# Kernel optimization log

Hardware: AMD Instinct MI355X
Metric: run time of the kernel (lower is better)

## Reference

```python
import jax, jax.numpy as jnp
import numpy as np


def setup_inputs() -> dict:
    key = jax.random.key(0)
    k1, k2, k3 = jax.random.split(key, 3)
    B, N, D = 512, 65536, 1          # batch, flattened heatmap locations (256x256), tag_dim
    P, K = 30, 17                    # max people, joints per person (COCO)
    tags = jax.random.normal(k1, (B, N, D), dtype=jnp.float32)
    idx = jax.random.randint(k2, (B, P, K), 0, N, dtype=jnp.int64)
    flag = (jax.random.uniform(k3, (B, P, K)) < 0.9).astype(jnp.int64)
    keypoints = jnp.stack([idx, flag], axis=-1)  # [B,P,K,2]
    return {"tags": tags, "keypoints": keypoints}


def reference(tags, keypoints):
    # tags: [B, N, D]; keypoints: [B, P, K, 2] int (flat_index, valid_flag)
    B, N, D = tags.shape
    _, P, K, _ = keypoints.shape
    idx = keypoints[..., 0]                               # [B,P,K]
    m = (keypoints[..., -1] == 1).astype(tags.dtype)      # [B,P,K] validity mask

    tags0 = tags[..., 0]                                  # [B,N] only channel 0 is used
    g = jnp.take_along_axis(tags0, idx.reshape(B, P * K), axis=1).reshape(B, P, K)

    cnt = m.sum(-1)                                       # [B,P] valid kpts per person
    safe_cnt = jnp.maximum(cnt, 1.0)
    mean = (g * m).sum(-1) / safe_cnt                     # [B,P] per-person mean tag

    # pull: mean squared deviation from person mean, averaged over valid people
    pull_p = (jnp.square(g - mean[..., None]) * m).sum(-1) / safe_cnt  # [B,P]
    pv = (cnt > 0).astype(tags.dtype)                     # [B,P] person valid
    n = pv.sum(-1)                                        # [B] valid people count
    pull = jnp.where(n > 0, (pull_p * pv).sum(-1) / jnp.maximum(n, 1.0), 0.0)

    # push: pairwise exp(-(mu_i - mu_j)^2) over valid-person pairs i<j
    diff = mean[:, :, None] - mean[:, None, :]            # [B,P,P]
    tri = jnp.triu(jnp.ones((P, P), dtype=tags.dtype), k=1)
    pair_m = pv[:, :, None] * pv[:, None, :] * tri        # [B,P,P]
    push_sum = (jnp.exp(-jnp.square(diff)) * pair_m).sum((-2, -1))  # [B]
    npairs = n * (n - 1.0) / 2.0
    push = jnp.where(n > 1, push_sum / jnp.maximum(npairs, 1.0), push_sum) * 0.5

    return jnp.stack([push, pull], axis=-1)               # [B,2]
```

## Files before the change

### kernel.cpp

```cpp
#include <hip/hip_runtime.h>

#define PP 30
#define KK 17
#define PK (PP * KK)

__global__ __launch_bounds__(64) void aeloss_kernel(
    const float* __restrict__ tags,
    const int*   __restrict__ kp,
    float*       __restrict__ out,
    int N)
{
    const int b = blockIdx.x;
    const int l = threadIdx.x;
    const int p    = l % PP;
    const int half = l / PP;
    const bool active = (l < 2 * PP);
    const int k0 = half ? 9 : 0;
    const int kn = half ? 8 : 9;

    const int*   kpb = kp   + (size_t)b * PK * 2;
    const float* tb  = tags + (size_t)b * N;

    int2 kv[9];
    #pragma unroll
    for (int k = 0; k < 9; ++k) {
        int kk = k0 + k; if (kk > KK - 1) kk = KK - 1;
        const int pp = active ? p : 0;
        kv[k] = *reinterpret_cast<const int2*>(kpb + (pp * KK + kk) * 2);
    }
    float g[9];
    #pragma unroll
    for (int k = 0; k < 9; ++k) g[k] = tb[kv[k].x];

    float s = 0.f, sq = 0.f, c = 0.f;
    #pragma unroll
    for (int k = 0; k < 9; ++k) {
        const float m = (active && (k < kn) && (kv[k].y == 1)) ? 1.f : 0.f;
        s  += g[k] * m;
        sq += g[k] * g[k] * m;
        c  += m;
    }

    s  += __shfl_down(s,  PP);
    sq += __shfl_down(sq, PP);
    c  += __shfl_down(c,  PP);

    float pv = 0.f, mean = 0.f, pullp = 0.f;
    if (l < PP) {
        pv = (c > 0.f) ? 1.f : 0.f;
        const float inv = 1.f / fmaxf(c, 1.f);
        mean  = s * inv;
        pullp = fmaxf(sq * inv - mean * mean, 0.f) * pv;
    }

    float row = 0.f;
    #pragma unroll
    for (int j = 1; j < PP; ++j) {
        const float meanj = __shfl(mean, j);
        const float pvj   = __shfl(pv,   j);
        const float d     = mean - meanj;
        row += (j > l) ? __expf(-d * d) * pvj * pv : 0.f;
    }

    float n = pv, pull_s = pullp, push_s = row;
    #pragma unroll
    for (int off = 16; off; off >>= 1) {
        n      += __shfl_down(n,      off);
        pull_s += __shfl_down(pull_s, off);
        push_s += __shfl_down(push_s, off);
    }

    if (l == 0) {
        const float pull   = (n > 0.f) ? (pull_s / fmaxf(n, 1.f)) : 0.f;
        const float npairs = n * (n - 1.f) * 0.5f;
        const float push   = ((n > 1.f) ? (push_s / fmaxf(npairs, 1.f)) : push_s) * 0.5f;
        out[b * 2 + 0] = push;
        out[b * 2 + 1] = pull;
    }
}

extern "C" void kernel_launch(void* const* d_in, const int* in_sizes, int n_in,
                              void* d_out, int out_size, void* d_ws, size_t ws_size,
                              hipStream_t stream) {
    const float* tags = (const float*)d_in[0];
    const int*   kp   = (const int*)d_in[1];
    float*       out  = (float*)d_out;

    const int B = out_size / 2;
    const int N = in_sizes[0] / B;

    aeloss_kernel<<<B, 64, 0, stream>>>(tags, kp, out, N);
}
```

Baseline: 9.942 us.

## Spread keypoint gathers across 512 threads with shared-memory per-person reduction

Each block now launches 512 threads, so every one of the 510 keypoints is gathered by its own thread and the loads go out in parallel. Before, 60 threads each issued 9 serialized dependent gathers. Masked values, squares and counts are staged in shared memory and one wavefront reduces them per person before the unchanged push/pull computation. This trades deeper per-thread memory latency chains for more threads, a block barrier and shared-memory traffic, and 7 of the 8 waves sit idle during the final stage.

```diff
diff --git a/kernel.cpp b/kernel.cpp
--- a/kernel.cpp
+++ b/kernel.cpp
@@ -4,78 +4,74 @@
 #define KK 17
 #define PK (PP * KK)
 
-__global__ __launch_bounds__(64) void aeloss_kernel(
+__global__ __launch_bounds__(512) void aeloss_kernel(
     const float* __restrict__ tags,
     const int*   __restrict__ kp,
     float*       __restrict__ out,
     int N)
 {
-    const int b = blockIdx.x;
-    const int l = threadIdx.x;
-    const int p    = l % PP;
-    const int half = l / PP;
-    const bool active = (l < 2 * PP);
-    const int k0 = half ? 9 : 0;
-    const int kn = half ? 8 : 9;
+    const int b   = blockIdx.x;
+    const int tid = threadIdx.x;
 
-    const int*   kpb = kp   + (size_t)b * PK * 2;
-    const float* tb  = tags + (size_t)b * N;
+    __shared__ float sA[PK];
+    __shared__ float sB[PK];
+    __shared__ float sC[PK];
 
-    int2 kv[9];
-    #pragma unroll
-    for (int k = 0; k < 9; ++k) {
-        int kk = k0 + k; if (kk > KK - 1) kk = KK - 1;
-        const int pp = active ? p : 0;
-        kv[k] = *reinterpret_cast<const int2*>(kpb + (pp * KK + kk) * 2);
+    if (tid < PK) {
+        const int2 kv = *reinterpret_cast<const int2*>(kp + ((size_t)b * PK + tid) * 2);
+        const float g = tags[(size_t)b * N + kv.x];
+        const float m = (kv.y == 1) ? 1.f : 0.f;
+        sA[tid] = g * m;
+        sB[tid] = g * g * m;
+        sC[tid] = m;
     }
-    float g[9];
-    #pragma unroll
-    for (int k = 0; k < 9; ++k) g[k] = tb[kv[k].x];
+    __syncthreads();
 
-    float s = 0.f, sq = 0.f, c = 0.f;
-    #pragma unroll
-    for (int k = 0; k < 9; ++k) {
-        const float m = (active && (k < kn) && (kv[k].y == 1)) ? 1.f : 0.f;
-        s  += g[k] * m;
-        sq += g[k] * g[k] * m;
-        c  += m;
-    }
+    if (tid < 64) {
+        const int l = tid;
+        float s = 0.f, sq = 0.f, c = 0.f;
+        if (l < PP) {
+            const int base = l * KK;
+            #pragma unroll
+            for (int k = 0; k < KK; ++k) {
+                s  += sA[base + k];
+                sq += sB[base + k];
+                c  += sC[base + k];
+            }
+        }
 
-    s  += __shfl_down(s,  PP);
-    sq += __shfl_down(sq, PP);
-    c  += __shfl_down(c,  PP);
+        float pv = 0.f, mean = 0.f, pullp = 0.f;
+        if (l < PP) {
+            pv = (c > 0.f) ? 1.f : 0.f;
+            const float inv = 1.f / fmaxf(c, 1.f);
+            mean  = s * inv;
+            pullp = fmaxf(sq * inv - mean * mean, 0.f) * pv;
+        }
 
-    float pv = 0.f, mean = 0.f, pullp = 0.f;
-    if (l < PP) {
-        pv = (c > 0.f) ? 1.f : 0.f;
-        const float inv = 1.f / fmaxf(c, 1.f);
-        mean  = s * inv;
-        pullp = fmaxf(sq * inv - mean * mean, 0.f) * pv;
-    }
+        float row = 0.f;
+        #pragma unroll
+        for (int j = 1; j < PP; ++j) {
+            const float meanj = __shfl(mean, j);
+            const float pvj   = __shfl(pv,   j);
+            const float d     = mean - meanj;
+            row += (j > l) ? __expf(-d * d) * pvj * pv : 0.f;
+        }
 
-    float row = 0.f;
-    #pragma unroll
-    for (int j = 1; j < PP; ++j) {
-        const float meanj = __shfl(mean, j);
-        const float pvj   = __shfl(pv,   j);
-        const float d     = mean - meanj;
-        row += (j > l) ? __expf(-d * d) * pvj * pv : 0.f;
-    }
+        float n = pv, pull_s = pullp, push_s = row;
+        #pragma unroll
+        for (int off = 16; off; off >>= 1) {
+            n      += __shfl_down(n,      off);
+            pull_s += __shfl_down(pull_s, off);
+            push_s += __shfl_down(push_s, off);
+        }
 
-    float n = pv, pull_s = pullp, push_s = row;
-    #pragma unroll
-    for (int off = 16; off; off >>= 1) {
-        n      += __shfl_down(n,      off);
-        pull_s += __shfl_down(pull_s, off);
-        push_s += __shfl_down(push_s, off);
-    }
-
-    if (l == 0) {
-        const float pull   = (n > 0.f) ? (pull_s / fmaxf(n, 1.f)) : 0.f;
-        const float npairs = n * (n - 1.f) * 0.5f;
-        const float push   = ((n > 1.f) ? (push_s / fmaxf(npairs, 1.f)) : push_s) * 0.5f;
-        out[b * 2 + 0] = push;
-        out[b * 2 + 1] = pull;
+        if (l == 0) {
+            const float pull   = (n > 0.f) ? (pull_s / fmaxf(n, 1.f)) : 0.f;
+            const float npairs = n * (n - 1.f) * 0.5f;
+            const float push   = ((n > 1.f) ? (push_s / fmaxf(npairs, 1.f)) : push_s) * 0.5f;
+            out[b * 2 + 0] = push;
+            out[b * 2 + 1] = pull;
+        }
     }
 }
 
@@ -89,5 +85,5 @@
     const int B = out_size / 2;
     const int N = in_sizes[0] / B;
 
-    aeloss_kernel<<<B, 64, 0, stream>>>(tags, kp, out, N);
+    aeloss_kernel<<<B, 512, 0, stream>>>(tags, kp, out, N);
 }
```

Result: no change. 9.878 us (-0.6%).
